# Kernel tuning notes

Measured on AMD Instinct MI355X. Metric: run time of the kernel, lower is better.

Reference implementation:

```python
import jax, jax.numpy as jnp
import numpy as np

# Module config (from init_kwargs)
HB, WB = 32, 32
FEATURE_SCALE = 1.0
# Input dims
B, C, HA, WA = 4, 64, 512, 512
N = 256


def setup_inputs() -> dict:
    key = jax.random.key(0)
    k1, k2, k3, k4 = jax.random.split(key, 4)
    aer_feat = jax.random.normal(k1, (B, C, HA, WA), dtype=jnp.float32)
    u = jax.random.uniform(k2, (B, N), minval=0.0, maxval=float(WA))
    v = jax.random.uniform(k3, (B, N), minval=0.0, maxval=float(HA))
    r = jax.random.uniform(k4, (B, N), minval=-np.pi, maxval=np.pi)
    pose_uvr = jnp.stack([u, v, r], axis=-1).astype(jnp.float32)
    return {"aer_feat": aer_feat, "pose_uvr": pose_uvr}


def _bilinear_sample(img, gx, gy):
    """grid_sample(mode='bilinear', padding_mode='zeros', align_corners=False)
    img: (C, Ha, Wa); gx, gy: (N, Hb, Wb) normalized coords in [-1, 1].
    Returns (C, N, Hb, Wb)."""
    Cc, Ha, Wa = img.shape
    # unnormalize (align_corners=False)
    ix = ((gx + 1.0) * Wa - 1.0) * 0.5
    iy = ((gy + 1.0) * Ha - 1.0) * 0.5
    x0 = jnp.floor(ix)
    y0 = jnp.floor(iy)
    x1 = x0 + 1.0
    y1 = y0 + 1.0
    wx1 = ix - x0
    wx0 = 1.0 - wx1
    wy1 = iy - y0
    wy0 = 1.0 - wy1
    flat = img.reshape(Cc, Ha * Wa)

    def gather(xc, yc, w):
        valid = (xc >= 0) & (xc < Wa) & (yc >= 0) & (yc < Ha)
        xi = jnp.clip(xc, 0, Wa - 1).astype(jnp.int32)
        yi = jnp.clip(yc, 0, Ha - 1).astype(jnp.int32)
        idx = (yi * Wa + xi).reshape(-1)
        vals = jnp.take(flat, idx, axis=1).reshape(Cc, *xc.shape)  # (C,N,Hb,Wb)
        return vals * (w * valid)[None]

    return (gather(x0, y0, wx0 * wy0) + gather(x1, y0, wx1 * wy0)
            + gather(x0, y1, wx0 * wy1) + gather(x1, y1, wx1 * wy1))


def reference(aer_feat, pose_uvr):
    Bb, Cc, Ha, Wa = aer_feat.shape
    # base grid: u rows flipped, v centered on Wb//2
    grid_u0 = jnp.broadcast_to(
        jnp.arange(HB - 1, -1, -1, dtype=jnp.float32)[:, None], (HB, WB))
    grid_v0 = jnp.broadcast_to(
        (jnp.arange(WB, dtype=jnp.float32) - WB // 2)[None, :], (HB, WB))
    u_off = pose_uvr[..., 0][..., None, None]  # (B,N,1,1)
    v_off = pose_uvr[..., 1][..., None, None]
    theta = pose_uvr[..., 2][..., None, None]
    cos_r = jnp.cos(-theta)
    sin_r = jnp.sin(-theta)
    gu = u_off + cos_r * grid_u0 - sin_r * grid_v0  # (B,N,Hb,Wb)
    gv = v_off + sin_r * grid_u0 + cos_r * grid_v0
    gx = (gu * FEATURE_SCALE + 0.5) * (2.0 / Wa) - 1.0
    gy = (gv * FEATURE_SCALE + 0.5) * (2.0 / Ha) - 1.0
    valid = (jnp.abs(gx) < 1.0) & (jnp.abs(gy) < 1.0)
    gx = jnp.where(valid, gx, 2.0)
    gy = jnp.where(valid, gy, 2.0)
    patches = jax.vmap(_bilinear_sample)(aer_feat, gx, gy)  # (B,C,N,Hb,Wb)
    return patches.transpose(0, 2, 1, 3, 4)  # (B,N,C,Hb,Wb)
```

## Files before the change

### kernel.cpp

```cpp
#include <hip/hip_runtime.h>

constexpr int HB_ = 32, WB_ = 32;
constexpr int HA_ = 512, WA_ = 512;
constexpr int C_  = 64,  N_  = 256;

constexpr int SH = 48;
constexpr int SCOLS = 48;
constexpr int SW = 49;
constexpr int PLANE = SH * SW;
constexpr int CPR = 4;
constexpr int KST = (SH * SCOLS) / 256;

__global__ __launch_bounds__(256, 4) void aps_kernel(
    const float* __restrict__ aer, const float* __restrict__ pose,
    float* __restrict__ out)
{
    __shared__ float lds[CPR * PLANE];

    const int bn  = blockIdx.x;
    const int b   = bn >> 8;
    const int tid = threadIdx.x;

    const float u  = pose[bn * 3 + 0];
    const float v  = pose[bn * 3 + 1];
    const float th = pose[bn * 3 + 2];
    float s_r, c_r;
    sincosf(-th, &s_r, &c_r);

    const float a00 = -s_r * -16.0f,              a01 = -s_r * 15.0f;
    const float a10 = c_r * 31.0f - s_r * -16.0f, a11 = c_r * 31.0f - s_r * 15.0f;
    const float gumin = u + fminf(fminf(a00, a01), fminf(a10, a11));
    const float b00 = c_r * -16.0f,               b01 = c_r * 15.0f;
    const float b10 = s_r * 31.0f + c_r * -16.0f, b11 = s_r * 31.0f + c_r * 15.0f;
    const float gvmin = v + fminf(fminf(b00, b01), fminf(b10, b11));
    const int x_lo = (int)floorf(gumin) - 1;
    const int y_lo = (int)floorf(gvmin) - 1;

    int   soff[KST]; int goff[KST]; float gmsk[KST];
    #pragma unroll
    for (int k = 0; k < KST; ++k) {
        const int e  = tid + 256 * k;
        const int r  = e / SCOLS;
        const int cl = e - r * SCOLS;
        const int y  = y_lo + r;
        const int x  = x_lo + cl;
        const bool ok = ((unsigned)y < (unsigned)HA_) && ((unsigned)x < (unsigned)WA_);
        soff[k] = r * SW + cl;
        goff[k] = ok ? (y * WA_ + x) : 0;
        gmsk[k] = ok ? 1.0f : 0.0f;
    }

    const int i  = tid >> 3;
    const int j0 = (tid & 7) * 4;
    const float gu_i = u + c_r * (float)(HB_ - 1 - i);
    const float gv_i = v + s_r * (float)(HB_ - 1 - i);

    int   lbase[4];
    float w[4][4];
    #pragma unroll
    for (int k = 0; k < 4; ++k) {
        const float gv0 = (float)(j0 + k - WB_ / 2);
        const float gu  = gu_i - s_r * gv0;
        const float gv  = gv_i + c_r * gv0;
        float gx = (gu + 0.5f) * (2.0f / (float)WA_) - 1.0f;
        float gy = (gv + 0.5f) * (2.0f / (float)HA_) - 1.0f;
        const bool valid = (fabsf(gx) < 1.0f) && (fabsf(gy) < 1.0f);
        if (!valid) { gx = 2.0f; gy = 2.0f; }
        const float ix = ((gx + 1.0f) * (float)WA_ - 1.0f) * 0.5f;
        const float iy = ((gy + 1.0f) * (float)HA_ - 1.0f) * 0.5f;
        const float x0f = floorf(ix), y0f = floorf(iy);
        const float wx1 = ix - x0f, wx0 = 1.0f - wx1;
        const float wy1 = iy - y0f, wy0 = 1.0f - wy1;
        const int x0 = (int)x0f, y0 = (int)y0f;
        const int x1 = x0 + 1,   y1 = y0 + 1;
        const bool vx0 = (x0 >= 0) & (x0 < WA_);
        const bool vx1 = (x1 >= 0) & (x1 < WA_);
        const bool vy0 = (y0 >= 0) & (y0 < HA_);
        const bool vy1 = (y1 >= 0) & (y1 < HA_);
        w[k][0] = wx0 * wy0 * ((vx0 && vy0) ? 1.0f : 0.0f);
        w[k][1] = wx1 * wy0 * ((vx1 && vy0) ? 1.0f : 0.0f);
        w[k][2] = wx0 * wy1 * ((vx0 && vy1) ? 1.0f : 0.0f);
        w[k][3] = wx1 * wy1 * ((vx1 && vy1) ? 1.0f : 0.0f);
        const int lx = min(max(x0 - x_lo, 0), SCOLS - 2);
        const int ly = min(max(y0 - y_lo, 0), SH - 2);
        lbase[k] = ly * SW + lx;
    }

    const float* img = aer + (size_t)b * C_ * (HA_ * WA_);
    float* op = out + (size_t)bn * C_ * (HB_ * WB_) + tid * 4;

    for (int c0 = 0; c0 < C_; c0 += CPR) {
        __syncthreads();
        #pragma unroll
        for (int cc = 0; cc < CPR; ++cc) {
            const float* im = img + (size_t)(c0 + cc) * (HA_ * WA_);
            float* pl = &lds[cc * PLANE];
            #pragma unroll
            for (int k = 0; k < KST; ++k)
                pl[soff[k]] = im[goff[k]] * gmsk[k];
        }
        __syncthreads();
        #pragma unroll
        for (int cc = 0; cc < CPR; ++cc) {
            const float* p = &lds[cc * PLANE];
            float rr[4];
            #pragma unroll
            for (int k = 0; k < 4; ++k) {
                const int lb = lbase[k];
                rr[k] = w[k][0] * p[lb]      + w[k][1] * p[lb + 1]
                      + w[k][2] * p[lb + SW] + w[k][3] * p[lb + SW + 1];
            }
            float4 r4; r4.x = rr[0]; r4.y = rr[1]; r4.z = rr[2]; r4.w = rr[3];
            *(float4*)(op + (size_t)(c0 + cc) * (HB_ * WB_)) = r4;
        }
    }
}

extern "C" void kernel_launch(void* const* d_in, const int* in_sizes, int n_in,
                              void* d_out, int out_size, void* d_ws, size_t ws_size,
                              hipStream_t stream) {
    const float* aer  = (const float*)d_in[0];
    const float* pose = (const float*)d_in[1];
    float* out = (float*)d_out;
    const int B = 4;
    aps_kernel<<<dim3(B * N_), dim3(256), 0, stream>>>(aer, pose, out);
}
```

Before: 486.3 us.

## Stage image tiles via direct global-to-LDS 16-byte loads and nontemporal output stores

```diff
diff --git a/kernel.cpp b/kernel.cpp
--- a/kernel.cpp
+++ b/kernel.cpp
@@ -4,12 +4,15 @@
 constexpr int HA_ = 512, WA_ = 512;
 constexpr int C_  = 64,  N_  = 256;
 
-constexpr int SH = 48;
-constexpr int SCOLS = 48;
-constexpr int SW = 49;
+constexpr int SH    = 48;
+constexpr int SCOLS = 52;
+constexpr int SW    = SCOLS;
+constexpr int GPROW = SCOLS / 4;
+constexpr int NGRP  = SH * GPROW;
 constexpr int PLANE = SH * SW;
-constexpr int CPR = 4;
-constexpr int KST = (SH * SCOLS) / 256;
+constexpr int CPR   = 4;
+
+typedef float f4v __attribute__((ext_vector_type(4)));
 
 __global__ __launch_bounds__(256, 4) void aps_kernel(
     const float* __restrict__ aer, const float* __restrict__ pose,
@@ -33,21 +36,20 @@
     const float b00 = c_r * -16.0f,               b01 = c_r * 15.0f;
     const float b10 = s_r * 31.0f + c_r * -16.0f, b11 = s_r * 31.0f + c_r * 15.0f;
     const float gvmin = v + fminf(fminf(b00, b01), fminf(b10, b11));
-    const int x_lo = (int)floorf(gumin) - 1;
-    const int y_lo = (int)floorf(gvmin) - 1;
+    const int x_lo  = (int)floorf(gumin) - 1;
+    const int y_lo  = (int)floorf(gvmin) - 1;
+    const int x_lo4 = x_lo & ~3;
 
-    int   soff[KST]; int goff[KST]; float gmsk[KST];
+    int goff[3];
     #pragma unroll
-    for (int k = 0; k < KST; ++k) {
-        const int e  = tid + 256 * k;
-        const int r  = e / SCOLS;
-        const int cl = e - r * SCOLS;
+    for (int k = 0; k < 3; ++k) {
+        const int g  = tid + 256 * k;
+        const int r  = g / GPROW;
+        const int c4 = g - r * GPROW;
         const int y  = y_lo + r;
-        const int x  = x_lo + cl;
+        const int x  = x_lo4 + c4 * 4;
         const bool ok = ((unsigned)y < (unsigned)HA_) && ((unsigned)x < (unsigned)WA_);
-        soff[k] = r * SW + cl;
         goff[k] = ok ? (y * WA_ + x) : 0;
-        gmsk[k] = ok ? 1.0f : 0.0f;
     }
 
     const int i  = tid >> 3;
@@ -81,7 +83,7 @@
         w[k][1] = wx1 * wy0 * ((vx1 && vy0) ? 1.0f : 0.0f);
         w[k][2] = wx0 * wy1 * ((vx0 && vy1) ? 1.0f : 0.0f);
         w[k][3] = wx1 * wy1 * ((vx1 && vy1) ? 1.0f : 0.0f);
-        const int lx = min(max(x0 - x_lo, 0), SCOLS - 2);
+        const int lx = min(max(x0 - x_lo4, 0), SCOLS - 2);
         const int ly = min(max(y0 - y_lo, 0), SH - 2);
         lbase[k] = ly * SW + lx;
     }
@@ -95,9 +97,20 @@
         for (int cc = 0; cc < CPR; ++cc) {
             const float* im = img + (size_t)(c0 + cc) * (HA_ * WA_);
             float* pl = &lds[cc * PLANE];
-            #pragma unroll
-            for (int k = 0; k < KST; ++k)
-                pl[soff[k]] = im[goff[k]] * gmsk[k];
+            __builtin_amdgcn_global_load_lds(
+                (const __attribute__((address_space(1))) unsigned int*)(im + goff[0]),
+                (__attribute__((address_space(3))) unsigned int*)(pl + tid * 4),
+                16, 0, 0);
+            __builtin_amdgcn_global_load_lds(
+                (const __attribute__((address_space(1))) unsigned int*)(im + goff[1]),
+                (__attribute__((address_space(3))) unsigned int*)(pl + (tid + 256) * 4),
+                16, 0, 0);
+            if (tid < NGRP - 512) {
+                __builtin_amdgcn_global_load_lds(
+                    (const __attribute__((address_space(1))) unsigned int*)(im + goff[2]),
+                    (__attribute__((address_space(3))) unsigned int*)(pl + (tid + 512) * 4),
+                    16, 0, 0);
+            }
         }
         __syncthreads();
         #pragma unroll
@@ -110,8 +123,9 @@
                 rr[k] = w[k][0] * p[lb]      + w[k][1] * p[lb + 1]
                       + w[k][2] * p[lb + SW] + w[k][3] * p[lb + SW + 1];
             }
-            float4 r4; r4.x = rr[0]; r4.y = rr[1]; r4.z = rr[2]; r4.w = rr[3];
-            *(float4*)(op + (size_t)(c0 + cc) * (HB_ * WB_)) = r4;
+            f4v r4 = {rr[0], rr[1], rr[2], rr[3]};
+            __builtin_nontemporal_store(r4,
+                (f4v*)(op + (size_t)(c0 + cc) * (HB_ * WB_)));
         }
     }
 }
```

Measured after the change: 467.0 us. -4.0%, faster.
